# Kernel optimization log

Hardware: AMD Instinct MI355X
Metric: run time of the kernel (lower is better)

## Reference

```python
import jax, jax.numpy as jnp
import numpy as np

D_MODEL = 512
NUM_HEADS = 8


def setup_inputs() -> dict:
    key = jax.random.key(0)
    ks = jax.random.split(key, 12)
    B, S, D = 2, 4096, D_MODEL
    scale = 1.0 / np.sqrt(D)
    inp = {
        "q": jax.random.normal(ks[0], (B, S, D), jnp.float32),
        "k": jax.random.normal(ks[1], (B, S, D), jnp.float32),
        "v": jax.random.normal(ks[2], (B, S, D), jnp.float32),
        "w_q": jax.random.normal(ks[3], (D, D), jnp.float32) * scale,
        "b_q": jax.random.normal(ks[4], (D,), jnp.float32) * scale,
        "w_k": jax.random.normal(ks[5], (D, D), jnp.float32) * scale,
        "b_k": jax.random.normal(ks[6], (D,), jnp.float32) * scale,
        "w_v": jax.random.normal(ks[7], (D, D), jnp.float32) * scale,
        "b_v": jax.random.normal(ks[8], (D,), jnp.float32) * scale,
        "w_o": jax.random.normal(ks[9], (D, D), jnp.float32) * scale,
        "b_o": jax.random.normal(ks[10], (D,), jnp.float32) * scale,
    }
    return inp


def _split_heads(x, h):
    b, s, d = x.shape
    return x.reshape(b, s, h, d // h).transpose(0, 2, 1, 3)  # [B,H,S,dk]


def reference(q, k, v, w_q, b_q, w_k, b_k, w_v, b_v, w_o, b_o):
    h = NUM_HEADS
    # Linear projections (torch Linear: x @ W.T + b)
    qh = _split_heads(q @ w_q.T + b_q, h)
    kh = _split_heads(k @ w_k.T + b_k, h)
    vh = _split_heads(v @ w_v.T + b_v, h)
    d_k = kh.shape[-1]
    scores = jnp.einsum("bhsd,bhtd->bhst", qh, kh) / jnp.sqrt(jnp.float32(d_k))
    attn = jax.nn.softmax(scores, axis=-1)  # [B,H,S,S] - materialized, as in source
    out = jnp.einsum("bhst,bhtd->bhsd", attn, vh)
    b, _, s, dk = out.shape
    out = out.transpose(0, 2, 1, 3).reshape(b, s, h * dk)
    return out @ w_o.T + b_o
```

## Files before the change

kernel.cpp:

```cpp
#include <hip/hip_runtime.h>
#include <hip/hip_bf16.h>

#define D_MODEL 512
#define NHEAD   8
#define DK      64
#define SEQ     4096
#define BATCH   2
#define NTOK    (BATCH * SEQ)

typedef __bf16 bf16;
typedef __bf16 bf16x4 __attribute__((ext_vector_type(4)));
typedef __bf16 bf16x8 __attribute__((ext_vector_type(8)));
typedef float  f32x4  __attribute__((ext_vector_type(4)));

#define MFMA16(a, b, c) __builtin_amdgcn_mfma_f32_16x16x32_bf16((a), (b), (c), 0, 0, 0)

#define QSCALE 0.18033688f

__global__ __launch_bounds__(256, 3) void proj_qkv(
    const float* __restrict__ q, const float* __restrict__ k, const float* __restrict__ v,
    const float* __restrict__ wq, const float* __restrict__ bq,
    const float* __restrict__ wk, const float* __restrict__ bk,
    const float* __restrict__ wv, const float* __restrict__ bv,
    bf16* __restrict__ Qh, bf16* __restrict__ Kh, bf16* __restrict__ Vt)
{
    const int p = blockIdx.z;
    const float* X    = (p == 0) ? q  : (p == 1) ? k  : v;
    const float* W    = (p == 0) ? wq : (p == 1) ? wk : wv;
    const float* bias = (p == 0) ? bq : (p == 1) ? bk : bv;

    __shared__ union __align__(16) {
        struct { bf16 As[128][72]; bf16 Bs[128][72]; } g;
        bf16 T[128][136];
    } sm;

    const int m0   = blockIdx.x * 128;
    const int n0   = blockIdx.y * 128;
    const int tid  = threadIdx.x;
    const int lane = tid & 63;
    const int wave = tid >> 6;
    const int low4 = lane & 15;
    const int quad = lane >> 4;
    const int wm   = wave >> 1;
    const int wn   = wave & 1;

    int srow[8], sc4[8];
    for (int it = 0; it < 8; ++it) {
        int idx = tid + it * 256;
        srow[it] = idx >> 4;
        sc4[it]  = (idx & 15) * 4;
    }

    float4 gA[8];
    for (int it = 0; it < 8; ++it)
        gA[it] = *(const float4*)(X + (size_t)(m0 + srow[it]) * D_MODEL + sc4[it]);

    f32x4 acc[4][4];
    for (int i = 0; i < 4; ++i)
        for (int j = 0; j < 4; ++j)
            acc[i][j] = f32x4{0.f, 0.f, 0.f, 0.f};

    for (int k0 = 0; k0 < D_MODEL; k0 += 64) {
        __syncthreads();
        for (int it = 0; it < 8; ++it) {
            bf16x4 wa = {(bf16)gA[it].x, (bf16)gA[it].y, (bf16)gA[it].z, (bf16)gA[it].w};
            *(bf16x4*)&sm.g.As[srow[it]][sc4[it]] = wa;
            float4 wv4 = *(const float4*)(W + (size_t)(n0 + srow[it]) * D_MODEL + k0 + sc4[it]);
            bf16x4 wb = {(bf16)wv4.x, (bf16)wv4.y, (bf16)wv4.z, (bf16)wv4.w};
            *(bf16x4*)&sm.g.Bs[srow[it]][sc4[it]] = wb;
        }
        __syncthreads();

        if (k0 + 64 < D_MODEL)
            for (int it = 0; it < 8; ++it)
                gA[it] = *(const float4*)(X + (size_t)(m0 + srow[it]) * D_MODEL + k0 + 64 + sc4[it]);

        for (int ks = 0; ks < 2; ++ks) {
            bf16x8 a[4], b[4];
            for (int i = 0; i < 4; ++i)
                a[i] = *(const bf16x8*)&sm.g.As[wm * 64 + i * 16 + low4][ks * 32 + quad * 8];
            for (int j = 0; j < 4; ++j)
                b[j] = *(const bf16x8*)&sm.g.Bs[wn * 64 + j * 16 + low4][ks * 32 + quad * 8];
            for (int i = 0; i < 4; ++i)
                for (int j = 0; j < 4; ++j)
                    acc[i][j] = MFMA16(a[i], b[j], acc[i][j]);
        }
    }

    if (p < 2) {
        bf16* Out = (p == 0) ? Qh : Kh;
        const float sc = (p == 0) ? QSCALE : 1.0f;
        for (int j = 0; j < 4; ++j) {
            int col = n0 + wn * 64 + j * 16 + low4;
            float bcol = bias[col];
            for (int i = 0; i < 4; ++i)
                for (int r = 0; r < 4; ++r) {
                    int row = m0 + wm * 64 + i * 16 + quad * 4 + r;
                    Out[(size_t)row * D_MODEL + col] = (bf16)((acc[i][j][r] + bcol) * sc);
                }
        }
    } else {
        __syncthreads();
        for (int j = 0; j < 4; ++j) {
            int col = n0 + wn * 64 + j * 16 + low4;
            float bcol = bias[col];
            for (int i = 0; i < 4; ++i)
                for (int r = 0; r < 4; ++r)
                    sm.T[wn * 64 + j * 16 + low4][wm * 64 + i * 16 + quad * 4 + r] =
                        (bf16)(acc[i][j][r] + bcol);
        }
        __syncthreads();
        const int bb = m0 >> 12;
        const int s0 = (m0 & 4095);
        for (int it = 0; it < 8; ++it) {
            int cc = it * 16 + (tid >> 4);
            int ml = (tid & 15) * 8;
            int col = n0 + cc;
            int hh = col >> 6, dd = col & 63;
            *(bf16x8*)&Vt[(((size_t)(bb * NHEAD + hh) * DK + dd) << 12) + s0 + ml] =
                *(const bf16x8*)&sm.T[cc][ml];
        }
    }
}

__global__ __launch_bounds__(512, 4) void attn(
    const bf16* __restrict__ Qh, const bf16* __restrict__ Kh,
    const bf16* __restrict__ Vt, bf16* __restrict__ O)
{
    __shared__ bf16 Ks[64][72];
    __shared__ bf16 Vs[64][72];
    __shared__ bf16 Ps[8][16][76];

    const int q0   = blockIdx.x * 128;
    const int bh   = blockIdx.y;
    const int b    = bh >> 3, h = bh & 7;
    const int tid  = threadIdx.x;
    const int lane = tid & 63;
    const int wave = tid >> 6;
    const int low4 = lane & 15;
    const int quad = lane >> 4;

    const bf16* Kbase = Kh + (size_t)b * SEQ * D_MODEL + h * DK;
    const bf16* Vbase = Vt + (size_t)bh * DK * SEQ;

    const int srow = tid >> 3;
    const int sg   = (tid & 7) * 8;

    const bf16* Qrow = Qh + (size_t)(b * SEQ + q0 + wave * 16 + low4) * D_MODEL + h * DK;
    bf16x8 qf0 = *(const bf16x8*)(Qrow + quad * 8);
    bf16x8 qf1 = *(const bf16x8*)(Qrow + 32 + quad * 8);

    float l = 0.f;
    f32x4 acc_o[4];
    for (int dt = 0; dt < 4; ++dt) acc_o[dt] = f32x4{0.f, 0.f, 0.f, 0.f};

    bf16x8 gk = *(const bf16x8*)(Kbase + (size_t)srow * D_MODEL + sg);
    bf16x8 gv = *(const bf16x8*)(Vbase + (size_t)srow * SEQ + sg);

    for (int t0 = 0; t0 < SEQ; t0 += 64) {
        __syncthreads();
        *(bf16x8*)&Ks[srow][sg] = gk;
        *(bf16x8*)&Vs[srow][sg] = gv;
        __syncthreads();

        bf16x8 kf[4][2], vf[4][2];
        for (int j = 0; j < 4; ++j)
            for (int ks = 0; ks < 2; ++ks) {
                kf[j][ks] = *(const bf16x8*)&Ks[j * 16 + low4][ks * 32 + quad * 8];
                vf[j][ks] = *(const bf16x8*)&Vs[j * 16 + low4][ks * 32 + quad * 8];
            }

        if (t0 + 64 < SEQ) {
            gk = *(const bf16x8*)(Kbase + (size_t)(t0 + 64 + srow) * D_MODEL + sg);
            gv = *(const bf16x8*)(Vbase + (size_t)srow * SEQ + t0 + 64 + sg);
        }

        f32x4 sc[4];
        for (int j = 0; j < 4; ++j) sc[j] = f32x4{0.f, 0.f, 0.f, 0.f};
        for (int ks = 0; ks < 2; ++ks)
            for (int j = 0; j < 4; ++j)
                sc[j] = MFMA16(kf[j][ks], qf1 * 0 + (ks ? qf1 : qf0), sc[j]);

        for (int j = 0; j < 4; ++j) {
            float p0 = __builtin_amdgcn_exp2f(sc[j][0]);
            float p1 = __builtin_amdgcn_exp2f(sc[j][1]);
            float p2 = __builtin_amdgcn_exp2f(sc[j][2]);
            float p3 = __builtin_amdgcn_exp2f(sc[j][3]);
            l += (p0 + p1) + (p2 + p3);
            bf16x4 pw = {(bf16)p0, (bf16)p1, (bf16)p2, (bf16)p3};
            *(bf16x4*)&Ps[wave][low4][j * 16 + quad * 4] = pw;
        }

        bf16x8 pf0 = *(const bf16x8*)&Ps[wave][low4][quad * 8];
        bf16x8 pf1 = *(const bf16x8*)&Ps[wave][low4][32 + quad * 8];
        for (int dt = 0; dt < 4; ++dt) {
            acc_o[dt] = MFMA16(pf0, vf[dt][0], acc_o[dt]);
            acc_o[dt] = MFMA16(pf1, vf[dt][1], acc_o[dt]);
        }
    }

    l += __shfl_xor(l, 16);
    l += __shfl_xor(l, 32);
    float inv = 1.0f / l;
    float invr[4];
    for (int r = 0; r < 4; ++r)
        invr[r] = __shfl(inv, quad * 4 + r);
    int rowb = b * SEQ + q0 + wave * 16;
    for (int dt = 0; dt < 4; ++dt)
        for (int r = 0; r < 4; ++r)
            O[(size_t)(rowb + quad * 4 + r) * D_MODEL + h * DK + dt * 16 + low4] =
                (bf16)(acc_o[dt][r] * invr[r]);
}

__global__ __launch_bounds__(256, 4) void proj_out(
    const bf16* __restrict__ Oin, const float* __restrict__ wo,
    const float* __restrict__ bo, float* __restrict__ out)
{
    __shared__ bf16 As[64][72];
    __shared__ bf16 Bs[64][72];

    const int m0   = blockIdx.x * 64;
    const int n0   = blockIdx.y * 64;
    const int tid  = threadIdx.x;
    const int lane = tid & 63;
    const int wave = tid >> 6;
    const int low4 = lane & 15;
    const int quad = lane >> 4;
    const int wm   = wave >> 1;
    const int wn   = wave & 1;

    int arow[2], ag[2];
    for (int it = 0; it < 2; ++it) {
        int idx = tid + it * 256;
        arow[it] = idx >> 3;
        ag[it]   = idx & 7;
    }
    int brow[4], bc4[4];
    for (int it = 0; it < 4; ++it) {
        int idx = tid + it * 256;
        brow[it] = idx >> 4;
        bc4[it]  = (idx & 15) * 4;
    }

    bf16x8 gA[2];
    float4 gB[4];
    for (int it = 0; it < 2; ++it)
        gA[it] = *(const bf16x8*)(Oin + (size_t)(m0 + arow[it]) * D_MODEL + ag[it] * 8);
    for (int it = 0; it < 4; ++it)
        gB[it] = *(const float4*)(wo + (size_t)(n0 + brow[it]) * D_MODEL + bc4[it]);

    f32x4 acc[2][2];
    for (int i = 0; i < 2; ++i)
        for (int j = 0; j < 2; ++j)
            acc[i][j] = f32x4{0.f, 0.f, 0.f, 0.f};

    for (int k0 = 0; k0 < D_MODEL; k0 += 64) {
        __syncthreads();
        for (int it = 0; it < 2; ++it)
            *(bf16x8*)&As[arow[it]][ag[it] * 8] = gA[it];
        for (int it = 0; it < 4; ++it) {
            bf16x4 wb = {(bf16)gB[it].x, (bf16)gB[it].y, (bf16)gB[it].z, (bf16)gB[it].w};
            *(bf16x4*)&Bs[brow[it]][bc4[it]] = wb;
        }
        __syncthreads();

        if (k0 + 64 < D_MODEL) {
            for (int it = 0; it < 2; ++it)
                gA[it] = *(const bf16x8*)(Oin + (size_t)(m0 + arow[it]) * D_MODEL + k0 + 64 + ag[it] * 8);
            for (int it = 0; it < 4; ++it)
                gB[it] = *(const float4*)(wo + (size_t)(n0 + brow[it]) * D_MODEL + k0 + 64 + bc4[it]);
        }

        for (int ks = 0; ks < 2; ++ks) {
            bf16x8 a[2], b[2];
            for (int i = 0; i < 2; ++i)
                a[i] = *(const bf16x8*)&As[wm * 32 + i * 16 + low4][ks * 32 + quad * 8];
            for (int j = 0; j < 2; ++j)
                b[j] = *(const bf16x8*)&Bs[wn * 32 + j * 16 + low4][ks * 32 + quad * 8];
            for (int i = 0; i < 2; ++i)
                for (int j = 0; j < 2; ++j)
                    acc[i][j] = MFMA16(a[i], b[j], acc[i][j]);
        }
    }

    for (int j = 0; j < 2; ++j) {
        int col = n0 + wn * 32 + j * 16 + low4;
        float bcol = bo[col];
        for (int i = 0; i < 2; ++i)
            for (int r = 0; r < 4; ++r) {
                int row = m0 + wm * 32 + i * 16 + quad * 4 + r;
                out[(size_t)row * D_MODEL + col] = acc[i][j][r] + bcol;
            }
    }
}

extern "C" void kernel_launch(void* const* d_in, const int* in_sizes, int n_in,
                              void* d_out, int out_size, void* d_ws, size_t ws_size,
                              hipStream_t stream)
{
    const float* q  = (const float*)d_in[0];
    const float* k  = (const float*)d_in[1];
    const float* v  = (const float*)d_in[2];
    const float* wq = (const float*)d_in[3];
    const float* bq = (const float*)d_in[4];
    const float* wk = (const float*)d_in[5];
    const float* bk = (const float*)d_in[6];
    const float* wv = (const float*)d_in[7];
    const float* bv = (const float*)d_in[8];
    const float* wo = (const float*)d_in[9];
    const float* bo = (const float*)d_in[10];

    const size_t NT = (size_t)NTOK * D_MODEL;
    bf16* Qh = (bf16*)d_ws;
    bf16* Kh = Qh + NT;
    bf16* Vt = Kh + NT;
    bf16* O  = Vt + NT;

    dim3 g1(NTOK / 128, D_MODEL / 128, 3);
    proj_qkv<<<g1, 256, 0, stream>>>(q, k, v, wq, bq, wk, bk, wv, bv, Qh, Kh, Vt);

    dim3 g2(SEQ / 128, BATCH * NHEAD);
    attn<<<g2, 512, 0, stream>>>(Qh, Kh, Vt, O);

    dim3 g3(NTOK / 64, D_MODEL / 64);
    proj_out<<<g3, 256, 0, stream>>>(O, wo, bo, (float*)d_out);
}
```

Measured before the change: 239.1 us.

## Use 32x32 MFMA with split-KV waves in attention and pre-convert weights to bf16

The attention kernel switches from 16x16x32 to 32x32x16 bf16 MFMA. Each block now processes 128 keys per iteration, split across two wave groups that are merged at the end through shared memory, which halves the number of barrier rounds and raises MFMA work per LDS load. A new small kernel converts all four weight matrices to bf16 once per call, so the projection kernels load bf16 weights directly instead of converting fp32 inside every tile. This adds one extra launch, a cross-wave reduction and more shared memory per attention block, which may lower occupancy.

Measured after the change: 231.8 us. -3.1%, faster.

```diff
diff --git a/kernel.cpp b/kernel.cpp
--- a/kernel.cpp
+++ b/kernel.cpp
@@ -12,21 +12,36 @@
 typedef __bf16 bf16x4 __attribute__((ext_vector_type(4)));
 typedef __bf16 bf16x8 __attribute__((ext_vector_type(8)));
 typedef float  f32x4  __attribute__((ext_vector_type(4)));
+typedef float  f32x16 __attribute__((ext_vector_type(16)));
 
 #define MFMA16(a, b, c) __builtin_amdgcn_mfma_f32_16x16x32_bf16((a), (b), (c), 0, 0, 0)
+#define MFMA32(a, b, c) __builtin_amdgcn_mfma_f32_32x32x16_bf16((a), (b), (c), 0, 0, 0)
 
 #define QSCALE 0.18033688f
+
+__global__ __launch_bounds__(256) void cvt_w(
+    const float* __restrict__ wq, const float* __restrict__ wk,
+    const float* __restrict__ wv, const float* __restrict__ wo,
+    bf16* __restrict__ Wb)
+{
+    int i = blockIdx.x * 256 + threadIdx.x;
+    int m = i >> 16;
+    int g = i & 65535;
+    const float* src = (m == 0) ? wq : (m == 1) ? wk : (m == 2) ? wv : wo;
+    float4 x = *(const float4*)(src + (size_t)g * 4);
+    bf16x4 y = {(bf16)x.x, (bf16)x.y, (bf16)x.z, (bf16)x.w};
+    *(bf16x4*)(Wb + (size_t)m * D_MODEL * D_MODEL + (size_t)g * 4) = y;
+}
 
 __global__ __launch_bounds__(256, 3) void proj_qkv(
     const float* __restrict__ q, const float* __restrict__ k, const float* __restrict__ v,
-    const float* __restrict__ wq, const float* __restrict__ bq,
-    const float* __restrict__ wk, const float* __restrict__ bk,
-    const float* __restrict__ wv, const float* __restrict__ bv,
+    const bf16* __restrict__ Wb,
+    const float* __restrict__ bq, const float* __restrict__ bk, const float* __restrict__ bv,
     bf16* __restrict__ Qh, bf16* __restrict__ Kh, bf16* __restrict__ Vt)
 {
     const int p = blockIdx.z;
     const float* X    = (p == 0) ? q  : (p == 1) ? k  : v;
-    const float* W    = (p == 0) ? wq : (p == 1) ? wk : wv;
+    const bf16*  W    = Wb + (size_t)p * D_MODEL * D_MODEL;
     const float* bias = (p == 0) ? bq : (p == 1) ? bk : bv;
 
     __shared__ union __align__(16) {
@@ -50,10 +65,19 @@
         srow[it] = idx >> 4;
         sc4[it]  = (idx & 15) * 4;
     }
+    int br[4], bc[4];
+    for (int it = 0; it < 4; ++it) {
+        int idx = tid + it * 256;
+        br[it] = idx >> 3;
+        bc[it] = (idx & 7) * 8;
+    }
 
     float4 gA[8];
+    bf16x8 gB[4];
     for (int it = 0; it < 8; ++it)
         gA[it] = *(const float4*)(X + (size_t)(m0 + srow[it]) * D_MODEL + sc4[it]);
+    for (int it = 0; it < 4; ++it)
+        gB[it] = *(const bf16x8*)(W + (size_t)(n0 + br[it]) * D_MODEL + bc[it]);
 
     f32x4 acc[4][4];
     for (int i = 0; i < 4; ++i)
@@ -65,15 +89,17 @@
         for (int it = 0; it < 8; ++it) {
             bf16x4 wa = {(bf16)gA[it].x, (bf16)gA[it].y, (bf16)gA[it].z, (bf16)gA[it].w};
             *(bf16x4*)&sm.g.As[srow[it]][sc4[it]] = wa;
-            float4 wv4 = *(const float4*)(W + (size_t)(n0 + srow[it]) * D_MODEL + k0 + sc4[it]);
-            bf16x4 wb = {(bf16)wv4.x, (bf16)wv4.y, (bf16)wv4.z, (bf16)wv4.w};
-            *(bf16x4*)&sm.g.Bs[srow[it]][sc4[it]] = wb;
-        }
-        __syncthreads();
-
-        if (k0 + 64 < D_MODEL)
+        }
+        for (int it = 0; it < 4; ++it)
+            *(bf16x8*)&sm.g.Bs[br[it]][bc[it]] = gB[it];
+        __syncthreads();
+
+        if (k0 + 64 < D_MODEL) {
             for (int it = 0; it < 8; ++it)
                 gA[it] = *(const float4*)(X + (size_t)(m0 + srow[it]) * D_MODEL + k0 + 64 + sc4[it]);
+            for (int it = 0; it < 4; ++it)
+                gB[it] = *(const bf16x8*)(W + (size_t)(n0 + br[it]) * D_MODEL + k0 + 64 + bc[it]);
+        }
 
         for (int ks = 0; ks < 2; ++ks) {
             bf16x8 a[4], b[4];
@@ -127,9 +153,12 @@
     const bf16* __restrict__ Qh, const bf16* __restrict__ Kh,
     const bf16* __restrict__ Vt, bf16* __restrict__ O)
 {
-    __shared__ bf16 Ks[64][72];
-    __shared__ bf16 Vs[64][72];
-    __shared__ bf16 Ps[8][16][76];
+    __shared__ union __align__(16) {
+        struct { bf16 Ks[128][72]; bf16 Vs[64][136]; } s;
+        float Obuf[4][32][68];
+    } sm;
+    __shared__ bf16  Ps[8][32][72];
+    __shared__ float Lbuf[4][32];
 
     const int q0   = blockIdx.x * 128;
     const int bh   = blockIdx.y;
@@ -137,83 +166,104 @@
     const int tid  = threadIdx.x;
     const int lane = tid & 63;
     const int wave = tid >> 6;
-    const int low4 = lane & 15;
-    const int quad = lane >> 4;
+    const int qg   = wave >> 1;
+    const int kg   = wave & 1;
+    const int m32  = lane & 31;
+    const int hl   = lane >> 5;
 
     const bf16* Kbase = Kh + (size_t)b * SEQ * D_MODEL + h * DK;
     const bf16* Vbase = Vt + (size_t)bh * DK * SEQ;
 
-    const int srow = tid >> 3;
-    const int sg   = (tid & 7) * 8;
-
-    const bf16* Qrow = Qh + (size_t)(b * SEQ + q0 + wave * 16 + low4) * D_MODEL + h * DK;
-    bf16x8 qf0 = *(const bf16x8*)(Qrow + quad * 8);
-    bf16x8 qf1 = *(const bf16x8*)(Qrow + 32 + quad * 8);
+    const bf16* Qrow = Qh + (size_t)(b * SEQ + q0 + qg * 32 + m32) * D_MODEL + h * DK;
+    bf16x8 qf[4];
+    for (int ks = 0; ks < 4; ++ks)
+        qf[ks] = *(const bf16x8*)(Qrow + ks * 16 + hl * 8);
 
     float l = 0.f;
-    f32x4 acc_o[4];
-    for (int dt = 0; dt < 4; ++dt) acc_o[dt] = f32x4{0.f, 0.f, 0.f, 0.f};
-
-    bf16x8 gk = *(const bf16x8*)(Kbase + (size_t)srow * D_MODEL + sg);
-    bf16x8 gv = *(const bf16x8*)(Vbase + (size_t)srow * SEQ + sg);
-
-    for (int t0 = 0; t0 < SEQ; t0 += 64) {
-        __syncthreads();
-        *(bf16x8*)&Ks[srow][sg] = gk;
-        *(bf16x8*)&Vs[srow][sg] = gv;
-        __syncthreads();
-
-        bf16x8 kf[4][2], vf[4][2];
-        for (int j = 0; j < 4; ++j)
-            for (int ks = 0; ks < 2; ++ks) {
-                kf[j][ks] = *(const bf16x8*)&Ks[j * 16 + low4][ks * 32 + quad * 8];
-                vf[j][ks] = *(const bf16x8*)&Vs[j * 16 + low4][ks * 32 + quad * 8];
-            }
-
-        if (t0 + 64 < SEQ) {
-            gk = *(const bf16x8*)(Kbase + (size_t)(t0 + 64 + srow) * D_MODEL + sg);
-            gv = *(const bf16x8*)(Vbase + (size_t)srow * SEQ + t0 + 64 + sg);
-        }
-
-        f32x4 sc[4];
-        for (int j = 0; j < 4; ++j) sc[j] = f32x4{0.f, 0.f, 0.f, 0.f};
-        for (int ks = 0; ks < 2; ++ks)
-            for (int j = 0; j < 4; ++j)
-                sc[j] = MFMA16(kf[j][ks], qf1 * 0 + (ks ? qf1 : qf0), sc[j]);
-
-        for (int j = 0; j < 4; ++j) {
-            float p0 = __builtin_amdgcn_exp2f(sc[j][0]);
-            float p1 = __builtin_amdgcn_exp2f(sc[j][1]);
-            float p2 = __builtin_amdgcn_exp2f(sc[j][2]);
-            float p3 = __builtin_amdgcn_exp2f(sc[j][3]);
-            l += (p0 + p1) + (p2 + p3);
-            bf16x4 pw = {(bf16)p0, (bf16)p1, (bf16)p2, (bf16)p3};
-            *(bf16x4*)&Ps[wave][low4][j * 16 + quad * 4] = pw;
-        }
-
-        bf16x8 pf0 = *(const bf16x8*)&Ps[wave][low4][quad * 8];
-        bf16x8 pf1 = *(const bf16x8*)&Ps[wave][low4][32 + quad * 8];
-        for (int dt = 0; dt < 4; ++dt) {
-            acc_o[dt] = MFMA16(pf0, vf[dt][0], acc_o[dt]);
-            acc_o[dt] = MFMA16(pf1, vf[dt][1], acc_o[dt]);
-        }
-    }
-
-    l += __shfl_xor(l, 16);
+    f32x16 acc[2];
+    for (int i = 0; i < 16; ++i) { acc[0][i] = 0.f; acc[1][i] = 0.f; }
+
+    int kr[2], kc[2], vr[2], vc[2];
+    for (int it = 0; it < 2; ++it) {
+        int c = tid + it * 512;
+        kr[it] = c >> 3;  kc[it] = (c & 7) * 8;
+        vr[it] = c >> 4;  vc[it] = (c & 15) * 8;
+    }
+    bf16x8 gk[2], gv[2];
+    for (int it = 0; it < 2; ++it) {
+        gk[it] = *(const bf16x8*)(Kbase + (size_t)kr[it] * D_MODEL + kc[it]);
+        gv[it] = *(const bf16x8*)(Vbase + (size_t)vr[it] * SEQ + vc[it]);
+    }
+
+    for (int t0 = 0; t0 < SEQ; t0 += 128) {
+        __syncthreads();
+        for (int it = 0; it < 2; ++it) {
+            *(bf16x8*)&sm.s.Ks[kr[it]][kc[it]] = gk[it];
+            *(bf16x8*)&sm.s.Vs[vr[it]][vc[it]] = gv[it];
+        }
+        __syncthreads();
+
+        if (t0 + 128 < SEQ) {
+            for (int it = 0; it < 2; ++it) {
+                gk[it] = *(const bf16x8*)(Kbase + (size_t)(t0 + 128 + kr[it]) * D_MODEL + kc[it]);
+                gv[it] = *(const bf16x8*)(Vbase + (size_t)vr[it] * SEQ + t0 + 128 + vc[it]);
+            }
+        }
+
+        for (int mt = 0; mt < 2; ++mt) {
+            f32x16 sc;
+            for (int i = 0; i < 16; ++i) sc[i] = 0.f;
+            for (int ks = 0; ks < 4; ++ks) {
+                bf16x8 kf = *(const bf16x8*)&sm.s.Ks[kg * 64 + mt * 32 + m32][ks * 16 + hl * 8];
+                sc = MFMA32(kf, qf[ks], sc);
+            }
+            for (int g = 0; g < 4; ++g) {
+                float p0 = __builtin_amdgcn_exp2f(sc[g * 4 + 0]);
+                float p1 = __builtin_amdgcn_exp2f(sc[g * 4 + 1]);
+                float p2 = __builtin_amdgcn_exp2f(sc[g * 4 + 2]);
+                float p3 = __builtin_amdgcn_exp2f(sc[g * 4 + 3]);
+                l += (p0 + p1) + (p2 + p3);
+                bf16x4 pw = {(bf16)p0, (bf16)p1, (bf16)p2, (bf16)p3};
+                *(bf16x4*)&Ps[wave][m32][mt * 32 + g * 8 + hl * 4] = pw;
+            }
+        }
+
+        for (int ks = 0; ks < 4; ++ks) {
+            bf16x8 pf = *(const bf16x8*)&Ps[wave][m32][ks * 16 + hl * 8];
+            for (int nt = 0; nt < 2; ++nt) {
+                bf16x8 vfr = *(const bf16x8*)&sm.s.Vs[nt * 32 + m32][kg * 64 + ks * 16 + hl * 8];
+                acc[nt] = MFMA32(pf, vfr, acc[nt]);
+            }
+        }
+    }
+
     l += __shfl_xor(l, 32);
-    float inv = 1.0f / l;
-    float invr[4];
-    for (int r = 0; r < 4; ++r)
-        invr[r] = __shfl(inv, quad * 4 + r);
-    int rowb = b * SEQ + q0 + wave * 16;
-    for (int dt = 0; dt < 4; ++dt)
-        for (int r = 0; r < 4; ++r)
-            O[(size_t)(rowb + quad * 4 + r) * D_MODEL + h * DK + dt * 16 + low4] =
-                (bf16)(acc_o[dt][r] * invr[r]);
+    __syncthreads();
+    if (kg == 1) {
+        for (int nt = 0; nt < 2; ++nt)
+            for (int r = 0; r < 16; ++r) {
+                int qq = (r & 3) + 8 * (r >> 2) + 4 * hl;
+                sm.Obuf[qg][qq][nt * 32 + m32] = acc[nt][r];
+            }
+        if (hl == 0) Lbuf[qg][m32] = l;
+    }
+    __syncthreads();
+    if (kg == 0) {
+        float lt  = l + Lbuf[qg][m32];
+        float inv = 1.0f / lt;
+        for (int nt = 0; nt < 2; ++nt)
+            for (int r = 0; r < 16; ++r) {
+                int qq = (r & 3) + 8 * (r >> 2) + 4 * hl;
+                float val = acc[nt][r] + sm.Obuf[qg][qq][nt * 32 + m32];
+                float iv  = __shfl(inv, qq);
+                O[(size_t)(b * SEQ + q0 + qg * 32 + qq) * D_MODEL + h * DK + nt * 32 + m32] =
+                    (bf16)(val * iv);
+            }
+    }
 }
 
 __global__ __launch_bounds__(256, 4) void proj_out(
-    const bf16* __restrict__ Oin, const float* __restrict__ wo,
+    const bf16* __restrict__ Oin, const bf16* __restrict__ Wo,
     const float* __restrict__ bo, float* __restrict__ out)
 {
     __shared__ bf16 As[64][72];
@@ -233,21 +283,14 @@
     for (int it = 0; it < 2; ++it) {
         int idx = tid + it * 256;
         arow[it] = idx >> 3;
-        ag[it]   = idx & 7;
-    }
-    int brow[4], bc4[4];
-    for (int it = 0; it < 4; ++it) {
-        int idx = tid + it * 256;
-        brow[it] = idx >> 4;
-        bc4[it]  = (idx & 15) * 4;
-    }
-
-    bf16x8 gA[2];
-    float4 gB[4];
-    for (int it = 0; it < 2; ++it)
-        gA[it] = *(const bf16x8*)(Oin + (size_t)(m0 + arow[it]) * D_MODEL + ag[it] * 8);
-    for (int it = 0; it < 4; ++it)
-        gB[it] = *(const float4*)(wo + (size_t)(n0 + brow[it]) * D_MODEL + bc4[it]);
+        ag[it]   = (idx & 7) * 8;
+    }
+
+    bf16x8 gA[2], gB[2];
+    for (int it = 0; it < 2; ++it) {
+        gA[it] = *(const bf16x8*)(Oin + (size_t)(m0 + arow[it]) * D_MODEL + ag[it]);
+        gB[it] = *(const bf16x8*)(Wo + (size_t)(n0 + arow[it]) * D_MODEL + ag[it]);
+    }
 
     f32x4 acc[2][2];
     for (int i = 0; i < 2; ++i)
@@ -256,19 +299,17 @@
 
     for (int k0 = 0; k0 < D_MODEL; k0 += 64) {
         __syncthreads();
-        for (int it = 0; it < 2; ++it)
-            *(bf16x8*)&As[arow[it]][ag[it] * 8] = gA[it];
-        for (int it = 0; it < 4; ++it) {
-            bf16x4 wb = {(bf16)gB[it].x, (bf16)gB[it].y, (bf16)gB[it].z, (bf16)gB[it].w};
-            *(bf16x4*)&Bs[brow[it]][bc4[it]] = wb;
+        for (int it = 0; it < 2; ++it) {
+            *(bf16x8*)&As[arow[it]][ag[it]] = gA[it];
+            *(bf16x8*)&Bs[arow[it]][ag[it]] = gB[it];
         }
         __syncthreads();
 
         if (k0 + 64 < D_MODEL) {
-            for (int it = 0; it < 2; ++it)
-                gA[it] = *(const bf16x8*)(Oin + (size_t)(m0 + arow[it]) * D_MODEL + k0 + 64 + ag[it] * 8);
-            for (int it = 0; it < 4; ++it)
-                gB[it] = *(const float4*)(wo + (size_t)(n0 + brow[it]) * D_MODEL + k0 + 64 + bc4[it]);
+            for (int it = 0; it < 2; ++it) {
+                gA[it] = *(const bf16x8*)(Oin + (size_t)(m0 + arow[it]) * D_MODEL + k0 + 64 + ag[it]);
+                gB[it] = *(const bf16x8*)(Wo + (size_t)(n0 + arow[it]) * D_MODEL + k0 + 64 + ag[it]);
+            }
         }
 
         for (int ks = 0; ks < 2; ++ks) {
@@ -315,13 +356,16 @@
     bf16* Kh = Qh + NT;
     bf16* Vt = Kh + NT;
     bf16* O  = Vt + NT;
+    bf16* Wb = O + NT;
+
+    cvt_w<<<1024, 256, 0, stream>>>(wq, wk, wv, wo, Wb);
 
     dim3 g1(NTOK / 128, D_MODEL / 128, 3);
-    proj_qkv<<<g1, 256, 0, stream>>>(q, k, v, wq, bq, wk, bk, wv, bv, Qh, Kh, Vt);
+    proj_qkv<<<g1, 256, 0, stream>>>(q, k, v, Wb, bq, bk, bv, Qh, Kh, Vt);
 
     dim3 g2(SEQ / 128, BATCH * NHEAD);
     attn<<<g2, 512, 0, stream>>>(Qh, Kh, Vt, O);
 
     dim3 g3(NTOK / 64, D_MODEL / 64);
-    proj_out<<<g3, 256, 0, stream>>>(O, wo, bo, (float*)d_out);
-}
+    proj_out<<<g3, 256, 0, stream>>>(O, Wb + (size_t)3 * D_MODEL * D_MODEL, bo, (float*)d_out);
+}
```
